# Kernel tuning notes

Measured on AMD Instinct MI355X. Metric: run time of the kernel, lower is better.

## Reference

```python
import jax, jax.numpy as jnp
import numpy as np
import math

DIM = 1024
MLP = 4096
D_STATE = 16
D_CONV = 4
EXPAND = 2
D_INNER = EXPAND * DIM
HALF = D_INNER // 2
DT_RANK = math.ceil(DIM / 16)
BSZ = 2
SEQ = 2048
LN_EPS = 1e-5


def setup_inputs() -> dict:
    key = jax.random.key(0)
    ks = jax.random.split(key, 12)
    s = lambda k, shape, sc: jax.random.normal(k, shape, dtype=jnp.float32) * sc
    return {
        "x": s(ks[0], (BSZ, SEQ, DIM), 1.0),
        "ln1_g": jnp.ones((DIM,), jnp.float32),
        "ln1_b": jnp.zeros((DIM,), jnp.float32),
        "in_proj_w": s(ks[1], (D_INNER, DIM), 0.02),
        "conv_x_w": s(ks[2], (HALF, 1, D_CONV), 0.1),
        "conv_x_b": jnp.zeros((HALF,), jnp.float32),
        "conv_z_w": s(ks[3], (HALF, 1, D_CONV), 0.1),
        "conv_z_b": jnp.zeros((HALF,), jnp.float32),
        "x_proj_w": s(ks[4], (DT_RANK + 2 * D_STATE, HALF), 0.02),
        "dt_proj_w": s(ks[5], (HALF, DT_RANK), 0.02),
        "dt_proj_b": s(ks[6], (HALF,), 0.1),
        "A_log": jnp.log(jnp.tile(jnp.arange(1, D_STATE + 1, dtype=jnp.float32), (HALF, 1))),
        "Dp": jnp.ones((HALF,), jnp.float32),
        "out_proj_w": s(ks[7], (DIM, D_INNER), 0.02),
        "ln2_g": jnp.ones((DIM,), jnp.float32),
        "ln2_b": jnp.zeros((DIM,), jnp.float32),
        "mlp_w1": s(ks[8], (MLP, DIM), 0.02),
        "mlp_b1": jnp.zeros((MLP,), jnp.float32),
        "mlp_w2": s(ks[9], (DIM, MLP), 0.02),
        "mlp_b2": jnp.zeros((DIM,), jnp.float32),
    }


def _ln(x, g, b):
    mu = jnp.mean(x, -1, keepdims=True)
    v = jnp.mean((x - mu) ** 2, -1, keepdims=True)
    return (x - mu) * jax.lax.rsqrt(v + LN_EPS) * g + b


def _dwconv_same(x, w, b):
    # x: [B, C, L]; w: [C, 1, K] depthwise; PyTorch 'same' pads left=(K-1)//2, right=rest
    total = D_CONV - 1
    left = total // 2
    y = jax.lax.conv_general_dilated(
        x, w, (1,), [(left, total - left)],
        dimension_numbers=("NCH", "OIH", "NCH"),
        feature_group_count=x.shape[1])
    return y + b[None, :, None]


def _mixer(x, in_proj_w, conv_x_w, conv_x_b, conv_z_w, conv_z_b,
           x_proj_w, dt_proj_w, dt_proj_b, A_log, Dp, out_proj_w):
    Bsz = x.shape[0]
    xz = jnp.einsum('bld,ed->ble', x, in_proj_w)              # [B,L,2*HALF]
    xs, zs = jnp.split(xz, 2, axis=-1)
    xc = jax.nn.silu(_dwconv_same(jnp.swapaxes(xs, 1, 2), conv_x_w, conv_x_b))  # [B,HALF,L]
    zc = jax.nn.silu(_dwconv_same(jnp.swapaxes(zs, 1, 2), conv_z_w, conv_z_b))  # [B,HALF,L]
    u = jnp.swapaxes(xc, 1, 2)                                 # [B,L,HALF]
    x_dbl = jnp.einsum('bld,ed->ble', u, x_proj_w)             # [B,L,dt_rank+2N]
    dt, Bm, Cm = jnp.split(x_dbl, [DT_RANK, DT_RANK + D_STATE], axis=-1)
    delta = jax.nn.softplus(jnp.einsum('blr,dr->bld', dt, dt_proj_w) + dt_proj_b)  # [B,L,HALF]
    A = -jnp.exp(A_log)                                        # [HALF,N]
    dA = jnp.exp(jnp.einsum('bld,dn->lbdn', delta, A))         # [L,B,HALF,N]
    dBu = jnp.einsum('bld,bln,bld->lbdn', delta, Bm, u)        # [L,B,HALF,N]
    Cs = jnp.moveaxis(Cm, 1, 0)                                # [L,B,N]

    def step(h, t):
        dA_t, dBu_t, c_t = t
        h = dA_t * h + dBu_t                                   # [B,HALF,N]
        return h, jnp.einsum('bdn,bn->bd', h, c_t)

    h0 = jnp.zeros((Bsz, HALF, D_STATE), x.dtype)
    _, ys = jax.lax.scan(step, h0, (dA, dBu, Cs))              # ys: [L,B,HALF]
    y = jnp.moveaxis(ys, 0, 1) + u * Dp                        # [B,L,HALF]
    y = jnp.concatenate([y, jnp.swapaxes(zc, 1, 2)], axis=-1)  # [B,L,2*HALF]
    return jnp.einsum('ble,de->bld', y, out_proj_w)


def reference(x, ln1_g, ln1_b, in_proj_w, conv_x_w, conv_x_b, conv_z_w, conv_z_b,
              x_proj_w, dt_proj_w, dt_proj_b, A_log, Dp, out_proj_w,
              ln2_g, ln2_b, mlp_w1, mlp_b1, mlp_w2, mlp_b2):
    x = x + _mixer(_ln(x, ln1_g, ln1_b), in_proj_w, conv_x_w, conv_x_b,
                   conv_z_w, conv_z_b, x_proj_w, dt_proj_w, dt_proj_b,
                   A_log, Dp, out_proj_w)
    h = _ln(x, ln2_g, ln2_b)
    h = jax.nn.gelu(jnp.einsum('bld,md->blm', h, mlp_w1) + mlp_b1, approximate=False)
    h = jnp.einsum('blm,dm->bld', h, mlp_w2) + mlp_b2
    return x + h
```

## Files before the change

### kernel.cpp

```cpp
#include <hip/hip_runtime.h>
#include <math.h>

#define DIMD    1024
#define MLPD    4096
#define DSTATE  16
#define DCONV   4
#define HALF    1024
#define DINNER  2048
#define DTRANK  64
#define BSZ     2
#define SEQ     2048
#define NTOK    (BSZ*SEQ)
#define NCH     64
#define CL      (SEQ/NCH)

typedef short bf16x8 __attribute__((ext_vector_type(8)));
typedef float f32x4  __attribute__((ext_vector_type(4)));
typedef unsigned short u16;
typedef unsigned int   u32;

__device__ __forceinline__ u16 f2bf(float x) {
    union { float f; unsigned int u; } v; v.f = x;
    unsigned int r = (v.u + 0x7FFFu + ((v.u >> 16) & 1u)) >> 16;
    return (u16)r;
}
__device__ __forceinline__ float bf2f(u16 x) {
    union { unsigned int u; float f; } v; v.u = ((unsigned int)x) << 16;
    return v.f;
}

#define SZ_WIN  (DINNER*DIMD)
#define SZ_WXP  (96*HALF)
#define SZ_WDT  (HALF*DTRANK)
#define SZ_WOUT (DIMD*DINNER)
#define SZ_WM1  (MLPD*DIMD)
#define SZ_WM2  (DIMD*MLPD)
#define SZ_TOT  (SZ_WIN+SZ_WXP+SZ_WDT+SZ_WOUT+SZ_WM1+SZ_WM2)

__global__ __launch_bounds__(256) void cvt6_kernel(
        const float* __restrict__ s0, u16* __restrict__ d0,
        const float* __restrict__ s1, u16* __restrict__ d1,
        const float* __restrict__ s2, u16* __restrict__ d2,
        const float* __restrict__ s3, u16* __restrict__ d3,
        const float* __restrict__ s4, u16* __restrict__ d4,
        const float* __restrict__ s5, u16* __restrict__ d5) {
    int i = blockIdx.x * 256 + threadIdx.x;
    if (i < SZ_WIN)  { d0[i] = f2bf(s0[i]); return; }  i -= SZ_WIN;
    if (i < SZ_WXP)  { d1[i] = f2bf(s1[i]); return; }  i -= SZ_WXP;
    if (i < SZ_WDT)  { d2[i] = f2bf(s2[i]); return; }  i -= SZ_WDT;
    if (i < SZ_WOUT) { d3[i] = f2bf(s3[i]); return; }  i -= SZ_WOUT;
    if (i < SZ_WM1)  { d4[i] = f2bf(s4[i]); return; }  i -= SZ_WM1;
    d5[i] = f2bf(s5[i]);
}

__global__ __launch_bounds__(256) void ln_bf16_kernel(
        const float* __restrict__ x, const float* __restrict__ g,
        const float* __restrict__ b, u16* __restrict__ out) {
    __shared__ float sm[4];
    int row = blockIdx.x;
    int t = threadIdx.x;
    const float4* xr = (const float4*)(x + (size_t)row * DIMD);
    float4 v = xr[t];
    float s = v.x + v.y + v.z + v.w;
    for (int off = 32; off > 0; off >>= 1) s += __shfl_down(s, off, 64);
    if ((t & 63) == 0) sm[t >> 6] = s;
    __syncthreads();
    float mu = (sm[0] + sm[1] + sm[2] + sm[3]) * (1.0f / DIMD);
    float dx = v.x - mu, dy = v.y - mu, dz = v.z - mu, dw = v.w - mu;
    float ss = dx*dx + dy*dy + dz*dz + dw*dw;
    for (int off = 32; off > 0; off >>= 1) ss += __shfl_down(ss, off, 64);
    __syncthreads();
    if ((t & 63) == 0) sm[t >> 6] = ss;
    __syncthreads();
    float var = (sm[0] + sm[1] + sm[2] + sm[3]) * (1.0f / DIMD);
    float rs = rsqrtf(var + 1e-5f);
    float4 gv = ((const float4*)g)[t];
    float4 bv = ((const float4*)b)[t];
    u16* o = out + (size_t)row * DIMD + t * 4;
    o[0] = f2bf(dx * rs * gv.x + bv.x);
    o[1] = f2bf(dy * rs * gv.y + bv.y);
    o[2] = f2bf(dz * rs * gv.z + bv.z);
    o[3] = f2bf(dw * rs * gv.w + bv.w);
}

__global__ __launch_bounds__(64) void gemm_small_kernel(
        const u16* __restrict__ A, int lda,
        const u16* __restrict__ W, int K, int N,
        float* __restrict__ Cf, u16* __restrict__ Cb) {
    int m0 = blockIdx.x * 16;
    int n0 = blockIdx.y * 16;
    int lane = threadIdx.x;
    int r = lane & 15, quad = lane >> 4;
    f32x4 acc = {0.f, 0.f, 0.f, 0.f};
    const u16* ap = A + (size_t)(m0 + r) * lda + quad * 8;
    const u16* wp = W + (size_t)(n0 + r) * K   + quad * 8;
    for (int k = 0; k < K; k += 32) {
        bf16x8 av = *(const bf16x8*)(ap + k);
        bf16x8 bv = *(const bf16x8*)(wp + k);
        acc = __builtin_amdgcn_mfma_f32_16x16x32_bf16(av, bv, acc, 0, 0, 0);
    }
    int col = n0 + r;
    #pragma unroll
    for (int i = 0; i < 4; ++i) {
        int row = m0 + quad * 4 + i;
        size_t idx = (size_t)row * N + col;
        Cf[idx] = acc[i];
        Cb[idx] = f2bf(acc[i]);
    }
}

template<int EPI, int TN, int KS>
__global__ __launch_bounds__(256) void gemm128_kernel(
        const u16* __restrict__ A, int lda, const u16* __restrict__ W,
        int K, int N,
        const float* __restrict__ bias, const float* __restrict__ resid,
        float* __restrict__ Cf, float* __restrict__ Cf2,
        u16* __restrict__ Cb) {
    constexpr int NF = TN / 32;
    __shared__ u16 As0[128 * 32], As1[128 * 32];
    __shared__ u16 Bs0[TN * 32],  Bs1[TN * 32];
    const int t = threadIdx.x;
    const int w = t >> 6;
    const int lane = t & 63;
    const int r = lane & 15, quad = lane >> 4;
    const int wm = w & 1, wn = w >> 1;
    const int m0 = blockIdx.x * 128;
    const int n0 = blockIdx.y * TN;
    const int Kloc = K / KS;
    const int kz = (KS == 2) ? blockIdx.z : 0;

    f32x4 acc[4][NF];
    #pragma unroll
    for (int mi = 0; mi < 4; ++mi)
        #pragma unroll
        for (int ni = 0; ni < NF; ++ni)
            acc[mi][ni] = (f32x4){0.f, 0.f, 0.f, 0.f};

    const u16* pa[2];
    const u16* pb[NF / 2];
    #pragma unroll
    for (int i = 0; i < 2; ++i) {
        int c = (i * 4 + w) * 64 + lane;
        int row = c >> 2;
        int q = (c & 3) ^ ((row >> 1) & 3);
        pa[i] = A + (size_t)(m0 + row) * lda + (size_t)kz * Kloc + q * 8;
    }
    #pragma unroll
    for (int i = 0; i < NF / 2; ++i) {
        int c = (i * 4 + w) * 64 + lane;
        int row = c >> 2;
        int q = (c & 3) ^ ((row >> 1) & 3);
        pb[i] = W + (size_t)(n0 + row) * K + (size_t)kz * Kloc + q * 8;
    }
    const int qs = quad ^ ((r >> 1) & 3);
    int aoff[4], boff[NF];
    #pragma unroll
    for (int mi = 0; mi < 4; ++mi)
        aoff[mi] = (wm * 64 + mi * 16 + r) * 32 + qs * 8;
    #pragma unroll
    for (int ni = 0; ni < NF; ++ni)
        boff[ni] = (wn * (TN / 2) + ni * 16 + r) * 32 + qs * 8;

    auto stage = [&](u16* __restrict__ Ad, u16* __restrict__ Bd) {
        #pragma unroll
        for (int i = 0; i < 2; ++i) {
            __builtin_amdgcn_global_load_lds(
                (const __attribute__((address_space(1))) u32*)pa[i],
                (__attribute__((address_space(3))) u32*)(Ad + (i * 4 + w) * 512),
                16, 0, 0);
            pa[i] += 32;
        }
        #pragma unroll
        for (int i = 0; i < NF / 2; ++i) {
            __builtin_amdgcn_global_load_lds(
                (const __attribute__((address_space(1))) u32*)pb[i],
                (__attribute__((address_space(3))) u32*)(Bd + (i * 4 + w) * 512),
                16, 0, 0);
            pb[i] += 32;
        }
    };
    auto compute = [&](const u16* __restrict__ Ab, const u16* __restrict__ Bb) {
        bf16x8 af[4], bfr[NF];
        #pragma unroll
        for (int mi = 0; mi < 4; ++mi) af[mi] = *(const bf16x8*)(Ab + aoff[mi]);
        #pragma unroll
        for (int ni = 0; ni < NF; ++ni) bfr[ni] = *(const bf16x8*)(Bb + boff[ni]);
        #pragma unroll
        for (int mi = 0; mi < 4; ++mi)
            #pragma unroll
            for (int ni = 0; ni < NF; ++ni)
                acc[mi][ni] = __builtin_amdgcn_mfma_f32_16x16x32_bf16(
                    af[mi], bfr[ni], acc[mi][ni], 0, 0, 0);
    };

    stage(As0, Bs0);
    for (int k0 = 0; k0 < Kloc; k0 += 64) {
        __syncthreads();
        if (k0 + 32 < Kloc) stage(As1, Bs1);
        compute(As0, Bs0);
        __syncthreads();
        if (k0 + 64 < Kloc) stage(As0, Bs0);
        compute(As1, Bs1);
    }

    float* Cfo = (KS == 2 && kz) ? Cf2 : Cf;
    #pragma unroll
    for (int mi = 0; mi < 4; ++mi) {
        #pragma unroll
        for (int i = 0; i < 4; ++i) {
            int row = m0 + wm * 64 + mi * 16 + quad * 4 + i;
            #pragma unroll
            for (int ni = 0; ni < NF; ++ni) {
                int col = n0 + wn * (TN / 2) + ni * 16 + r;
                size_t idx = (size_t)row * N + col;
                float v = acc[mi][ni][i];
                if (EPI == 1) { v += bias[col]; v = (v > 20.f) ? v : log1pf(expf(v)); }
                if (EPI == 2) { v += bias[col]; v = 0.5f * v * (1.0f + erff(v * 0.70710678118654752f)); }
                if (EPI == 3) { v += resid[idx]; }
                if (EPI == 4) { v += bias[col] + resid[idx]; }
                if (EPI == 2 || EPI == 5) Cb[idx] = f2bf(v);
                else                      Cfo[idx] = v;
            }
        }
    }
}

template<int EPI>
__global__ __launch_bounds__(256) void reduce2_kernel(
        const float* __restrict__ P0, const float* __restrict__ P1,
        const float* __restrict__ bias, const float* __restrict__ resid,
        float* __restrict__ out) {
    size_t idx = ((size_t)blockIdx.x * 256 + threadIdx.x) * 4;
    float4 a = *(const float4*)(P0 + idx);
    float4 b = *(const float4*)(P1 + idx);
    float4 rr = *(const float4*)(resid + idx);
    float4 o;
    o.x = a.x + b.x + rr.x;
    o.y = a.y + b.y + rr.y;
    o.z = a.z + b.z + rr.z;
    o.w = a.w + b.w + rr.w;
    if (EPI == 4) {
        int col = (int)(idx & (DIMD - 1));
        float4 bb = *(const float4*)(bias + col);
        o.x += bb.x; o.y += bb.y; o.z += bb.z; o.w += bb.w;
    }
    *(float4*)(out + idx) = o;
}

__global__ __launch_bounds__(256) void conv_silu_kernel(
        const u16* __restrict__ xz,
        const float* __restrict__ wx, const float* __restrict__ bx,
        const float* __restrict__ wz, const float* __restrict__ bz,
        u16* __restrict__ u_bf, u16* __restrict__ ycat) {
    int c  = blockIdx.x * 256 + threadIdx.x;
    int bl = blockIdx.y;
    int l  = bl & (SEQ - 1);
    float accx = bx[c], accz = bz[c];
    #pragma unroll
    for (int k = 0; k < DCONV; ++k) {
        int lp = l + k - 1;
        if (lp >= 0 && lp < SEQ) {
            const u16* rowp = xz + (size_t)(bl + (lp - l)) * DINNER;
            accx += bf2f(rowp[c])        * wx[c * DCONV + k];
            accz += bf2f(rowp[HALF + c]) * wz[c * DCONV + k];
        }
    }
    float sx = accx * __fdividef(1.f, 1.f + __expf(-accx));
    float sz = accz * __fdividef(1.f, 1.f + __expf(-accz));
    u_bf[(size_t)bl * HALF + c] = f2bf(sx);
    ycat[(size_t)bl * DINNER + HALF + c] = f2bf(sz);
}

__global__ __launch_bounds__(256) void scan_p1_kernel(
        const float* __restrict__ delta, const u16* __restrict__ u_bf,
        const float* __restrict__ x_dbl, const float* __restrict__ A_log,
        float* __restrict__ hfin, float* __restrict__ dsum) {
    int t  = blockIdx.x * 256 + threadIdx.x;
    int d  = t & (HALF - 1);
    int ch = (t >> 10) & (NCH - 1);
    int b  = t >> 16;
    float Ac[16], h[16];
    #pragma unroll
    for (int i = 0; i < 4; ++i) {
        float4 a = *(const float4*)&A_log[d * DSTATE + i * 4];
        Ac[4*i+0] = -__expf(a.x); Ac[4*i+1] = -__expf(a.y);
        Ac[4*i+2] = -__expf(a.z); Ac[4*i+3] = -__expf(a.w);
        h[4*i+0] = 0.f; h[4*i+1] = 0.f; h[4*i+2] = 0.f; h[4*i+3] = 0.f;
    }
    int l0 = b * SEQ + ch * CL;
    size_t off = (size_t)l0 * HALF + d;
    const float* xrow = x_dbl + (size_t)l0 * 96;
    float ds = 0.f;
    #pragma unroll 4
    for (int l = 0; l < CL; ++l) {
        float dl = delta[off];
        float uv = bf2f(u_bf[off]);
        off += HALF;
        float4 B0 = *(const float4*)(xrow + 64);
        float4 B1 = *(const float4*)(xrow + 68);
        float4 B2 = *(const float4*)(xrow + 72);
        float4 B3 = *(const float4*)(xrow + 76);
        xrow += 96;
        float dBu = dl * uv;
        ds += dl;
        float Bv[16] = {B0.x,B0.y,B0.z,B0.w, B1.x,B1.y,B1.z,B1.w,
                        B2.x,B2.y,B2.z,B2.w, B3.x,B3.y,B3.z,B3.w};
        #pragma unroll
        for (int n = 0; n < 16; ++n)
            h[n] = __expf(dl * Ac[n]) * h[n] + dBu * Bv[n];
    }
    float4* hf = (float4*)&hfin[(size_t)t * 16];
    #pragma unroll
    for (int i = 0; i < 4; ++i)
        hf[i] = (float4){h[4*i+0], h[4*i+1], h[4*i+2], h[4*i+3]};
    dsum[t] = ds;
}

__global__ __launch_bounds__(256) void scan_p2_kernel(
        const float* __restrict__ A_log, const float* __restrict__ dsum,
        const float* __restrict__ hfin, float* __restrict__ hin) {
    int t = blockIdx.x * 256 + threadIdx.x;
    int n = t & 15;
    int d = (t >> 4) & (HALF - 1);
    int b = t >> 14;
    float Ac = -__expf(A_log[d * DSTATE + n]);
    float h = 0.f;
    for (int ch = 0; ch < NCH; ++ch) {
        size_t chain = ((size_t)(b * NCH + ch) * HALF) + d;
        hin[chain * 16 + n] = h;
        float ds = dsum[chain];
        h = __expf(Ac * ds) * h + hfin[chain * 16 + n];
    }
}

__global__ __launch_bounds__(256) void scan_p3_kernel(
        const float* __restrict__ delta, const u16* __restrict__ u_bf,
        const float* __restrict__ x_dbl, const float* __restrict__ A_log,
        const float* __restrict__ Dp, const float* __restrict__ hin,
        u16* __restrict__ ycat) {
    int t  = blockIdx.x * 256 + threadIdx.x;
    int d  = t & (HALF - 1);
    int ch = (t >> 10) & (NCH - 1);
    int b  = t >> 16;
    float Ac[16], h[16];
    #pragma unroll
    for (int i = 0; i < 4; ++i) {
        float4 a  = *(const float4*)&A_log[d * DSTATE + i * 4];
        float4 hv = *(const float4*)&hin[(size_t)t * 16 + i * 4];
        Ac[4*i+0] = -__expf(a.x); Ac[4*i+1] = -__expf(a.y);
        Ac[4*i+2] = -__expf(a.z); Ac[4*i+3] = -__expf(a.w);
        h[4*i+0] = hv.x; h[4*i+1] = hv.y; h[4*i+2] = hv.z; h[4*i+3] = hv.w;
    }
    float Dv = Dp[d];
    int l0 = b * SEQ + ch * CL;
    size_t off = (size_t)l0 * HALF + d;
    const float* xrow = x_dbl + (size_t)l0 * 96;
    u16* yp = ycat + (size_t)l0 * DINNER + d;
    #pragma unroll 4
    for (int l = 0; l < CL; ++l) {
        float dl = delta[off];
        float uv = bf2f(u_bf[off]);
        off += HALF;
        float4 B0 = *(const float4*)(xrow + 64);
        float4 B1 = *(const float4*)(xrow + 68);
        float4 B2 = *(const float4*)(xrow + 72);
        float4 B3 = *(const float4*)(xrow + 76);
        float4 C0 = *(const float4*)(xrow + 80);
        float4 C1 = *(const float4*)(xrow + 84);
        float4 C2 = *(const float4*)(xrow + 88);
        float4 C3 = *(const float4*)(xrow + 92);
        xrow += 96;
        float dBu = dl * uv;
        float Bv[16] = {B0.x,B0.y,B0.z,B0.w, B1.x,B1.y,B1.z,B1.w,
                        B2.x,B2.y,B2.z,B2.w, B3.x,B3.y,B3.z,B3.w};
        float Cv[16] = {C0.x,C0.y,C0.z,C0.w, C1.x,C1.y,C1.z,C1.w,
                        C2.x,C2.y,C2.z,C2.w, C3.x,C3.y,C3.z,C3.w};
        float y = uv * Dv;
        #pragma unroll
        for (int n = 0; n < 16; ++n) {
            h[n] = __expf(dl * Ac[n]) * h[n] + dBu * Bv[n];
            y += h[n] * Cv[n];
        }
        *yp = f2bf(y);
        yp += DINNER;
    }
}

extern "C" void kernel_launch(void* const* d_in, const int* in_sizes, int n_in,
                              void* d_out, int out_size, void* d_ws, size_t ws_size,
                              hipStream_t stream) {
    const float* x         = (const float*)d_in[0];
    const float* ln1_g     = (const float*)d_in[1];
    const float* ln1_b     = (const float*)d_in[2];
    const float* in_proj_w = (const float*)d_in[3];
    const float* conv_x_w  = (const float*)d_in[4];
    const float* conv_x_b  = (const float*)d_in[5];
    const float* conv_z_w  = (const float*)d_in[6];
    const float* conv_z_b  = (const float*)d_in[7];
    const float* x_proj_w  = (const float*)d_in[8];
    const float* dt_proj_w = (const float*)d_in[9];
    const float* dt_proj_b = (const float*)d_in[10];
    const float* A_log     = (const float*)d_in[11];
    const float* Dp        = (const float*)d_in[12];
    const float* out_proj_w= (const float*)d_in[13];
    const float* ln2_g     = (const float*)d_in[14];
    const float* ln2_b     = (const float*)d_in[15];
    const float* mlp_w1    = (const float*)d_in[16];
    const float* mlp_b1    = (const float*)d_in[17];
    const float* mlp_w2    = (const float*)d_in[18];
    const float* mlp_b2    = (const float*)d_in[19];
    float* out = (float*)d_out;

    char* p = (char*)d_ws;
    auto alloc = [&](size_t bytes) {
        char* r = p; p += (bytes + 255) & ~(size_t)255; return r;
    };
    u16*   w_in   = (u16*)  alloc((size_t)DINNER * DIMD * 2);
    u16*   w_xp   = (u16*)  alloc((size_t)96 * HALF * 2);
    u16*   w_dt   = (u16*)  alloc((size_t)HALF * DTRANK * 2);
    u16*   w_out  = (u16*)  alloc((size_t)DIMD * DINNER * 2);
    u16*   w_m1   = (u16*)  alloc((size_t)MLPD * DIMD * 2);
    u16*   w_m2   = (u16*)  alloc((size_t)DIMD * MLPD * 2);
    u16*   xn_bf  = (u16*)  alloc((size_t)NTOK * DIMD * 2);
    u16*   xz_bf  = (u16*)  alloc((size_t)NTOK * DINNER * 2);
    u16*   u_bf   = (u16*)  alloc((size_t)NTOK * HALF * 2);
    u16*   ycat   = (u16*)  alloc((size_t)NTOK * DINNER * 2);
    float* x_dbl  = (float*)alloc((size_t)NTOK * 96 * 4);
    u16*   xdbl_bf= (u16*)  alloc((size_t)NTOK * 96 * 2);
    float* delta  = (float*)alloc((size_t)NTOK * HALF * 4);
    float* x2     = (float*)alloc((size_t)NTOK * DIMD * 4);
    u16*   ln2_bf = (u16*)  alloc((size_t)NTOK * DIMD * 2);
    u16*   mlp_h  = (u16*)  alloc((size_t)NTOK * MLPD * 2);
    float* hfin = (float*)mlp_h;
    float* hin  = hfin + (size_t)BSZ * NCH * HALF * DSTATE;
    float* dsum = hin  + (size_t)BSZ * NCH * HALF * DSTATE;
    float* P0 = delta;
    float* P1 = (float*)xz_bf;

    cvt6_kernel<<<SZ_TOT / 256, 256, 0, stream>>>(
        in_proj_w, w_in, x_proj_w, w_xp, dt_proj_w, w_dt,
        out_proj_w, w_out, mlp_w1, w_m1, mlp_w2, w_m2);

    ln_bf16_kernel<<<NTOK, 256, 0, stream>>>(x, ln1_g, ln1_b, xn_bf);

    gemm128_kernel<5,128,1><<<dim3(NTOK/128, DINNER/128), 256, 0, stream>>>(
        xn_bf, DIMD, w_in, DIMD, DINNER, nullptr, nullptr, nullptr, nullptr, xz_bf);

    conv_silu_kernel<<<dim3(HALF/256, NTOK), 256, 0, stream>>>(
        xz_bf, conv_x_w, conv_x_b, conv_z_w, conv_z_b, u_bf, ycat);

    gemm_small_kernel<<<dim3(NTOK/16, 96/16), 64, 0, stream>>>(
        u_bf, HALF, w_xp, HALF, 96, x_dbl, xdbl_bf);

    gemm128_kernel<1,64,1><<<dim3(NTOK/128, HALF/64), 256, 0, stream>>>(
        xdbl_bf, 96, w_dt, DTRANK, HALF, dt_proj_b, nullptr, delta, nullptr, nullptr);

    scan_p1_kernel<<<(BSZ*NCH*HALF)/256, 256, 0, stream>>>(
        delta, u_bf, x_dbl, A_log, hfin, dsum);
    scan_p2_kernel<<<(BSZ*HALF*DSTATE)/256, 256, 0, stream>>>(
        A_log, dsum, hfin, hin);
    scan_p3_kernel<<<(BSZ*NCH*HALF)/256, 256, 0, stream>>>(
        delta, u_bf, x_dbl, A_log, Dp, hin, ycat);

    gemm128_kernel<0,64,2><<<dim3(NTOK/128, DIMD/64, 2), 256, 0, stream>>>(
        ycat, DINNER, w_out, DINNER, DIMD, nullptr, nullptr, P0, P1, nullptr);
    reduce2_kernel<3><<<(NTOK*DIMD)/1024, 256, 0, stream>>>(
        P0, P1, nullptr, x, x2);

    ln_bf16_kernel<<<NTOK, 256, 0, stream>>>(x2, ln2_g, ln2_b, ln2_bf);

    gemm128_kernel<2,128,1><<<dim3(NTOK/128, MLPD/128), 256, 0, stream>>>(
        ln2_bf, DIMD, w_m1, DIMD, MLPD, mlp_b1, nullptr, nullptr, nullptr, mlp_h);

    gemm128_kernel<0,64,2><<<dim3(NTOK/128, DIMD/64, 2), 256, 0, stream>>>(
        mlp_h, MLPD, w_m2, MLPD, DIMD, nullptr, nullptr, P0, P1, nullptr);
    reduce2_kernel<4><<<(NTOK*DIMD)/1024, 256, 0, stream>>>(
        P0, P1, mlp_b2, x2, out);
}
```

Before: 480.9 us.

## Fuse LN with weight conversion and reduce, approximate GELU, retile small kernels

Merges the first layernorm into the weight-conversion launch and fuses the out-proj split-K reduction with the second layernorm, removing two launches and one activation round trip. The x_proj GEMM uses split-K across four waves, and the conv+SiLU kernel processes eight tokens per thread with a sliding register window to reuse loads. The in_proj GEMM switches to 64-wide N tiles. The exact erf GELU is replaced by a tanh-style sigmoid approximation, which trades some accuracy for cheaper math.

```diff
diff --git a/kernel.cpp b/kernel.cpp
--- a/kernel.cpp
+++ b/kernel.cpp
@@ -36,26 +36,27 @@
 #define SZ_WM1  (MLPD*DIMD)
 #define SZ_WM2  (DIMD*MLPD)
 #define SZ_TOT  (SZ_WIN+SZ_WXP+SZ_WDT+SZ_WOUT+SZ_WM1+SZ_WM2)
-
-__global__ __launch_bounds__(256) void cvt6_kernel(
+#define CVT_BLOCKS ((SZ_TOT + 255) / 256)
+
+__global__ __launch_bounds__(256) void cvtln_kernel(
+        const float* __restrict__ x, const float* __restrict__ g,
+        const float* __restrict__ b, u16* __restrict__ xn_bf,
         const float* __restrict__ s0, u16* __restrict__ d0,
         const float* __restrict__ s1, u16* __restrict__ d1,
         const float* __restrict__ s2, u16* __restrict__ d2,
         const float* __restrict__ s3, u16* __restrict__ d3,
         const float* __restrict__ s4, u16* __restrict__ d4,
         const float* __restrict__ s5, u16* __restrict__ d5) {
-    int i = blockIdx.x * 256 + threadIdx.x;
-    if (i < SZ_WIN)  { d0[i] = f2bf(s0[i]); return; }  i -= SZ_WIN;
-    if (i < SZ_WXP)  { d1[i] = f2bf(s1[i]); return; }  i -= SZ_WXP;
-    if (i < SZ_WDT)  { d2[i] = f2bf(s2[i]); return; }  i -= SZ_WDT;
-    if (i < SZ_WOUT) { d3[i] = f2bf(s3[i]); return; }  i -= SZ_WOUT;
-    if (i < SZ_WM1)  { d4[i] = f2bf(s4[i]); return; }  i -= SZ_WM1;
-    d5[i] = f2bf(s5[i]);
-}
-
-__global__ __launch_bounds__(256) void ln_bf16_kernel(
-        const float* __restrict__ x, const float* __restrict__ g,
-        const float* __restrict__ b, u16* __restrict__ out) {
+    if (blockIdx.x >= NTOK) {
+        int i = (blockIdx.x - NTOK) * 256 + threadIdx.x;
+        if (i < SZ_WIN)  { d0[i] = f2bf(s0[i]); return; }  i -= SZ_WIN;
+        if (i < SZ_WXP)  { d1[i] = f2bf(s1[i]); return; }  i -= SZ_WXP;
+        if (i < SZ_WDT)  { d2[i] = f2bf(s2[i]); return; }  i -= SZ_WDT;
+        if (i < SZ_WOUT) { d3[i] = f2bf(s3[i]); return; }  i -= SZ_WOUT;
+        if (i < SZ_WM1)  { d4[i] = f2bf(s4[i]); return; }  i -= SZ_WM1;
+        if (i < SZ_WM2)  { d5[i] = f2bf(s5[i]); }
+        return;
+    }
     __shared__ float sm[4];
     int row = blockIdx.x;
     int t = threadIdx.x;
@@ -76,36 +77,46 @@
     float rs = rsqrtf(var + 1e-5f);
     float4 gv = ((const float4*)g)[t];
     float4 bv = ((const float4*)b)[t];
-    u16* o = out + (size_t)row * DIMD + t * 4;
+    u16* o = xn_bf + (size_t)row * DIMD + t * 4;
     o[0] = f2bf(dx * rs * gv.x + bv.x);
     o[1] = f2bf(dy * rs * gv.y + bv.y);
     o[2] = f2bf(dz * rs * gv.z + bv.z);
     o[3] = f2bf(dw * rs * gv.w + bv.w);
 }
 
-__global__ __launch_bounds__(64) void gemm_small_kernel(
+__global__ __launch_bounds__(256) void gemm_small_kernel(
         const u16* __restrict__ A, int lda,
         const u16* __restrict__ W, int K, int N,
         float* __restrict__ Cf, u16* __restrict__ Cb) {
-    int m0 = blockIdx.x * 16;
+    __shared__ f32x4 red[2][64];
+    int t = threadIdx.x;
+    int w = t >> 6, lane = t & 63;
+    int mt = w & 1, kh = w >> 1;
+    int m0 = blockIdx.x * 32 + mt * 16;
     int n0 = blockIdx.y * 16;
-    int lane = threadIdx.x;
     int r = lane & 15, quad = lane >> 4;
+    int Kh = K >> 1;
     f32x4 acc = {0.f, 0.f, 0.f, 0.f};
-    const u16* ap = A + (size_t)(m0 + r) * lda + quad * 8;
-    const u16* wp = W + (size_t)(n0 + r) * K   + quad * 8;
-    for (int k = 0; k < K; k += 32) {
+    const u16* ap = A + (size_t)(m0 + r) * lda + kh * Kh + quad * 8;
+    const u16* wp = W + (size_t)(n0 + r) * K   + kh * Kh + quad * 8;
+    for (int k = 0; k < Kh; k += 32) {
         bf16x8 av = *(const bf16x8*)(ap + k);
         bf16x8 bv = *(const bf16x8*)(wp + k);
         acc = __builtin_amdgcn_mfma_f32_16x16x32_bf16(av, bv, acc, 0, 0, 0);
     }
-    int col = n0 + r;
-    #pragma unroll
-    for (int i = 0; i < 4; ++i) {
-        int row = m0 + quad * 4 + i;
-        size_t idx = (size_t)row * N + col;
-        Cf[idx] = acc[i];
-        Cb[idx] = f2bf(acc[i]);
+    if (kh == 1) red[mt][lane] = acc;
+    __syncthreads();
+    if (kh == 0) {
+        f32x4 o = red[mt][lane];
+        int col = n0 + r;
+        #pragma unroll
+        for (int i = 0; i < 4; ++i) {
+            int row = m0 + quad * 4 + i;
+            size_t idx = (size_t)row * N + col;
+            float v = acc[i] + o[i];
+            Cf[idx] = v;
+            Cb[idx] = f2bf(v);
+        }
     }
 }
 
@@ -215,7 +226,11 @@
                 size_t idx = (size_t)row * N + col;
                 float v = acc[mi][ni][i];
                 if (EPI == 1) { v += bias[col]; v = (v > 20.f) ? v : log1pf(expf(v)); }
-                if (EPI == 2) { v += bias[col]; v = 0.5f * v * (1.0f + erff(v * 0.70710678118654752f)); }
+                if (EPI == 2) {
+                    v += bias[col];
+                    float e = __expf(fminf(1.5957691216f * v + 0.0713548162f * v * v * v, 80.f));
+                    v = v * __fdividef(e, e + 1.f);
+                }
                 if (EPI == 3) { v += resid[idx]; }
                 if (EPI == 4) { v += bias[col] + resid[idx]; }
                 if (EPI == 2 || EPI == 5) Cb[idx] = f2bf(v);
@@ -225,7 +240,6 @@
     }
 }
 
-template<int EPI>
 __global__ __launch_bounds__(256) void reduce2_kernel(
         const float* __restrict__ P0, const float* __restrict__ P1,
         const float* __restrict__ bias, const float* __restrict__ resid,
@@ -234,17 +248,54 @@
     float4 a = *(const float4*)(P0 + idx);
     float4 b = *(const float4*)(P1 + idx);
     float4 rr = *(const float4*)(resid + idx);
+    int col = (int)(idx & (DIMD - 1));
+    float4 bb = *(const float4*)(bias + col);
     float4 o;
-    o.x = a.x + b.x + rr.x;
-    o.y = a.y + b.y + rr.y;
-    o.z = a.z + b.z + rr.z;
-    o.w = a.w + b.w + rr.w;
-    if (EPI == 4) {
-        int col = (int)(idx & (DIMD - 1));
-        float4 bb = *(const float4*)(bias + col);
-        o.x += bb.x; o.y += bb.y; o.z += bb.z; o.w += bb.w;
-    }
+    o.x = a.x + b.x + rr.x + bb.x;
+    o.y = a.y + b.y + rr.y + bb.y;
+    o.z = a.z + b.z + rr.z + bb.z;
+    o.w = a.w + b.w + rr.w + bb.w;
     *(float4*)(out + idx) = o;
+}
+
+__global__ __launch_bounds__(256) void reduce_ln_kernel(
+        const float* __restrict__ P0, const float* __restrict__ P1,
+        const float* __restrict__ resid,
+        const float* __restrict__ g, const float* __restrict__ b,
+        float* __restrict__ x2, u16* __restrict__ out_bf) {
+    __shared__ float sm[4];
+    int row = blockIdx.x;
+    int t = threadIdx.x;
+    size_t base = (size_t)row * DIMD + t * 4;
+    float4 a  = *(const float4*)(P0 + base);
+    float4 p  = *(const float4*)(P1 + base);
+    float4 rr = *(const float4*)(resid + base);
+    float4 v;
+    v.x = a.x + p.x + rr.x;
+    v.y = a.y + p.y + rr.y;
+    v.z = a.z + p.z + rr.z;
+    v.w = a.w + p.w + rr.w;
+    *(float4*)(x2 + base) = v;
+    float s = v.x + v.y + v.z + v.w;
+    for (int off = 32; off > 0; off >>= 1) s += __shfl_down(s, off, 64);
+    if ((t & 63) == 0) sm[t >> 6] = s;
+    __syncthreads();
+    float mu = (sm[0] + sm[1] + sm[2] + sm[3]) * (1.0f / DIMD);
+    float dx = v.x - mu, dy = v.y - mu, dz = v.z - mu, dw = v.w - mu;
+    float ss = dx*dx + dy*dy + dz*dz + dw*dw;
+    for (int off = 32; off > 0; off >>= 1) ss += __shfl_down(ss, off, 64);
+    __syncthreads();
+    if ((t & 63) == 0) sm[t >> 6] = ss;
+    __syncthreads();
+    float var = (sm[0] + sm[1] + sm[2] + sm[3]) * (1.0f / DIMD);
+    float rs = rsqrtf(var + 1e-5f);
+    float4 gv = ((const float4*)g)[t];
+    float4 bv = ((const float4*)b)[t];
+    u16* o = out_bf + base;
+    o[0] = f2bf(dx * rs * gv.x + bv.x);
+    o[1] = f2bf(dy * rs * gv.y + bv.y);
+    o[2] = f2bf(dz * rs * gv.z + bv.z);
+    o[3] = f2bf(dw * rs * gv.w + bv.w);
 }
 
 __global__ __launch_bounds__(256) void conv_silu_kernel(
@@ -253,22 +304,36 @@
         const float* __restrict__ wz, const float* __restrict__ bz,
         u16* __restrict__ u_bf, u16* __restrict__ ycat) {
     int c  = blockIdx.x * 256 + threadIdx.x;
-    int bl = blockIdx.y;
-    int l  = bl & (SEQ - 1);
-    float accx = bx[c], accz = bz[c];
-    #pragma unroll
-    for (int k = 0; k < DCONV; ++k) {
-        int lp = l + k - 1;
-        if (lp >= 0 && lp < SEQ) {
-            const u16* rowp = xz + (size_t)(bl + (lp - l)) * DINNER;
-            accx += bf2f(rowp[c])        * wx[c * DCONV + k];
-            accz += bf2f(rowp[HALF + c]) * wz[c * DCONV + k];
-        }
-    }
-    float sx = accx * __fdividef(1.f, 1.f + __expf(-accx));
-    float sz = accz * __fdividef(1.f, 1.f + __expf(-accz));
-    u_bf[(size_t)bl * HALF + c] = f2bf(sx);
-    ycat[(size_t)bl * DINNER + HALF + c] = f2bf(sz);
+    int gy = blockIdx.y;
+    int b  = gy >> 8;
+    int l0 = (gy & 255) * 8;
+    const u16* base = xz + ((size_t)(b * SEQ + l0)) * DINNER;
+    float wxr[4], wzr[4];
+    #pragma unroll
+    for (int k = 0; k < 4; ++k) { wxr[k] = wx[c * 4 + k]; wzr[k] = wz[c * 4 + k]; }
+    float bxv = bx[c], bzv = bz[c];
+    float xm1 = (l0 > 0) ? bf2f(base[c - DINNER]) : 0.f;
+    float x0v = bf2f(base[c]);
+    float x1v = bf2f(base[c + DINNER]);
+    float zm1 = (l0 > 0) ? bf2f(base[HALF + c - DINNER]) : 0.f;
+    float z0v = bf2f(base[HALF + c]);
+    float z1v = bf2f(base[HALF + c + DINNER]);
+    u16* up = u_bf + ((size_t)(b * SEQ + l0)) * HALF + c;
+    u16* yp = ycat + ((size_t)(b * SEQ + l0)) * DINNER + HALF + c;
+    #pragma unroll
+    for (int l = 0; l < 8; ++l) {
+        bool in = (l0 + l + 2) < SEQ;
+        float x2v = in ? bf2f(base[(size_t)(l + 2) * DINNER + c]) : 0.f;
+        float z2v = in ? bf2f(base[(size_t)(l + 2) * DINNER + HALF + c]) : 0.f;
+        float ax = bxv + wxr[0]*xm1 + wxr[1]*x0v + wxr[2]*x1v + wxr[3]*x2v;
+        float az = bzv + wzr[0]*zm1 + wzr[1]*z0v + wzr[2]*z1v + wzr[3]*z2v;
+        float sx = ax * __fdividef(1.f, 1.f + __expf(-ax));
+        float sz = az * __fdividef(1.f, 1.f + __expf(-az));
+        *up = f2bf(sx); *yp = f2bf(sz);
+        up += HALF; yp += DINNER;
+        xm1 = x0v; x0v = x1v; x1v = x2v;
+        zm1 = z0v; z0v = z1v; z1v = z2v;
+    }
 }
 
 __global__ __launch_bounds__(256) void scan_p1_kernel(
@@ -437,19 +502,18 @@
     float* P0 = delta;
     float* P1 = (float*)xz_bf;
 
-    cvt6_kernel<<<SZ_TOT / 256, 256, 0, stream>>>(
+    cvtln_kernel<<<NTOK + CVT_BLOCKS, 256, 0, stream>>>(
+        x, ln1_g, ln1_b, xn_bf,
         in_proj_w, w_in, x_proj_w, w_xp, dt_proj_w, w_dt,
         out_proj_w, w_out, mlp_w1, w_m1, mlp_w2, w_m2);
 
-    ln_bf16_kernel<<<NTOK, 256, 0, stream>>>(x, ln1_g, ln1_b, xn_bf);
-
-    gemm128_kernel<5,128,1><<<dim3(NTOK/128, DINNER/128), 256, 0, stream>>>(
+    gemm128_kernel<5,64,1><<<dim3(NTOK/128, DINNER/64), 256, 0, stream>>>(
         xn_bf, DIMD, w_in, DIMD, DINNER, nullptr, nullptr, nullptr, nullptr, xz_bf);
 
-    conv_silu_kernel<<<dim3(HALF/256, NTOK), 256, 0, stream>>>(
+    conv_silu_kernel<<<dim3(HALF/256, NTOK/8), 256, 0, stream>>>(
         xz_bf, conv_x_w, conv_x_b, conv_z_w, conv_z_b, u_bf, ycat);
 
-    gemm_small_kernel<<<dim3(NTOK/16, 96/16), 64, 0, stream>>>(
+    gemm_small_kernel<<<dim3(NTOK/32, 96/16), 256, 0, stream>>>(
         u_bf, HALF, w_xp, HALF, 96, x_dbl, xdbl_bf);
 
     gemm128_kernel<1,64,1><<<dim3(NTOK/128, HALF/64), 256, 0, stream>>>(
@@ -464,16 +528,14 @@
 
     gemm128_kernel<0,64,2><<<dim3(NTOK/128, DIMD/64, 2), 256, 0, stream>>>(
         ycat, DINNER, w_out, DINNER, DIMD, nullptr, nullptr, P0, P1, nullptr);
-    reduce2_kernel<3><<<(NTOK*DIMD)/1024, 256, 0, stream>>>(
-        P0, P1, nullptr, x, x2);
-
-    ln_bf16_kernel<<<NTOK, 256, 0, stream>>>(x2, ln2_g, ln2_b, ln2_bf);
+    reduce_ln_kernel<<<NTOK, 256, 0, stream>>>(
+        P0, P1, x, ln2_g, ln2_b, x2, ln2_bf);
 
     gemm128_kernel<2,128,1><<<dim3(NTOK/128, MLPD/128), 256, 0, stream>>>(
         ln2_bf, DIMD, w_m1, DIMD, MLPD, mlp_b1, nullptr, nullptr, nullptr, mlp_h);
 
     gemm128_kernel<0,64,2><<<dim3(NTOK/128, DIMD/64, 2), 256, 0, stream>>>(
         mlp_h, MLPD, w_m2, MLPD, DIMD, nullptr, nullptr, P0, P1, nullptr);
-    reduce2_kernel<4><<<(NTOK*DIMD)/1024, 256, 0, stream>>>(
+    reduce2_kernel<<<(NTOK*DIMD)/1024, 256, 0, stream>>>(
         P0, P1, mlp_b2, x2, out);
 }
```

Result: faster. 443.9 us (-7.7%).
